# Kernel tuning notes

Hardware: AMD Instinct MI355X
Metric: run time of the kernel (lower is better)

Reference implementation:

```python
import jax, jax.numpy as jnp
import numpy as np

U, I, D = 100000, 200000, 64   # users, items, emb_size
N = U + I                      # total nodes
NNZ = 6400000                  # adjacency non-zeros
B = 4096                       # batch of (user,item) pairs
L = 3                          # n_layers


def setup_inputs() -> dict:
    key = jax.random.key(0)
    ks = jax.random.split(key, 11)
    s = 1.0 / np.sqrt(D)  # xavier-ish scale
    return {
        "user_emb_online": jax.random.normal(ks[0], (U, D), jnp.float32) * s,
        "item_emb_online": jax.random.normal(ks[1], (I, D), jnp.float32) * s,
        "user_emb_target": jax.random.normal(ks[2], (U, D), jnp.float32) * s,
        "item_emb_target": jax.random.normal(ks[3], (I, D), jnp.float32) * s,
        # normalized adjacency values (positive, roughly 1/deg scale)
        "adj_val": jax.random.uniform(ks[4], (NNZ,), jnp.float32) * (1.0 / 16.0),
        "pred_w": jax.random.normal(ks[5], (D, D), jnp.float32) * s,
        "pred_b": jnp.zeros((D,), jnp.float32),
        "adj_row": jax.random.randint(ks[6], (NNZ,), 0, N, dtype=jnp.int32),
        "adj_col": jax.random.randint(ks[7], (NNZ,), 0, N, dtype=jnp.int32),
        "user_idx": jax.random.randint(ks[8], (B,), 0, U, dtype=jnp.int32),
        "item_idx": jax.random.randint(ks[9], (B,), 0, I, dtype=jnp.int32),
    }


def _spmm(row, col, val, x):
    # sparse [N,N] @ dense [N,D] via gather + segment-sum
    return jax.ops.segment_sum(val[:, None] * x[col], row, num_segments=N)


def _lgcn_encode(user_emb, item_emb, row, col, val):
    ego = jnp.concatenate([user_emb, item_emb], axis=0)  # [N, D]
    acc = ego
    x = ego
    for _ in range(L):
        x = _spmm(row, col, val, x)
        acc = acc + x
    all_emb = acc / (L + 1)  # mean over stacked layer outputs
    return all_emb[:U], all_emb[U:]


def reference(user_emb_online, item_emb_online, user_emb_target, item_emb_target,
              adj_val, pred_w, pred_b, adj_row, adj_col, user_idx, item_idx):
    u_on_all, i_on_all = _lgcn_encode(user_emb_online, item_emb_online, adj_row, adj_col, adj_val)
    u_tg_all, i_tg_all = _lgcn_encode(user_emb_target, item_emb_target, adj_row, adj_col, adj_val)
    u_online = u_on_all[user_idx]   # [B, D]
    i_online = i_on_all[item_idx]
    u_target = u_tg_all[user_idx]
    i_target = i_tg_all[item_idx]
    u_pred = u_online @ pred_w.T + pred_b  # nn.Linear
    i_pred = i_online @ pred_w.T + pred_b
    return (u_pred, u_target, i_pred, i_target)
```

## Files before the change

### kernel.cpp

```cpp
#include <hip/hip_runtime.h>
#include <hip/hip_bf16.h>
#include <stdint.h>

#define U_N   100000
#define I_N   200000
#define NN    300000
#define DD    64
#define NNZ_N 6400000
#define BB    4096
#define CHUNK 4096
#define NB    ((NN + CHUNK - 1) / CHUNK)
#define NBK   74
#define EPB   4096
#define NSB   1184
#define SUBCAP 6656
#define BKCAP  94208
#define BKBLK  23
#define LBLK   48000

typedef unsigned short u16;
typedef unsigned int   u32;
typedef float vf2 __attribute__((ext_vector_type(2)));

__device__ __forceinline__ u16 f2bf(float f) {
    u32 u = __float_as_uint(f);
    u32 r = (u + 0x7FFFu + ((u >> 16) & 1u)) >> 16;
    return (u16)r;
}


#if __has_builtin(__builtin_amdgcn_cvt_pk_f32_fp8) && __has_builtin(__builtin_amdgcn_cvt_pk_fp8_f32)
#define FP8_HW 1
#else
#define FP8_HW 0
#endif

__device__ __forceinline__ u32 enc1_fp8(float f) {
    float af = fabsf(f);
    u32 s = (__float_as_uint(f) >> 31) << 7;
    if (af >= 0.015625f) {
        u32 au = __float_as_uint(af);
        u32 r = au + 0x7FFFFu + ((au >> 20) & 1u);
        u32 e = (r >> 23) - 120u;
        u32 m = (r >> 20) & 7u;
        if (e > 15u) { e = 15u; m = 6u; }
        return s | (e << 3) | m;
    } else {
        u32 q = (u32)__float2int_rn(af * 512.0f);
        return s | q;
    }
}

__device__ __forceinline__ u32 pack4_fp8(float a, float b, float c, float d) {
#if FP8_HW
    u32 w = 0;
    w = (u32)__builtin_amdgcn_cvt_pk_fp8_f32(a, b, (int)w, false);
    w = (u32)__builtin_amdgcn_cvt_pk_fp8_f32(c, d, (int)w, true);
    return w;
#else
    return enc1_fp8(a) | (enc1_fp8(b) << 8) | (enc1_fp8(c) << 16) | (enc1_fp8(d) << 24);
#endif
}

__device__ __forceinline__ float dec1_fp8(u32 b) {
    u32 s = (b & 0x80u) << 24;
    u32 e = (b >> 3) & 15u;
    u32 m = b & 7u;
    float mag = e ? __uint_as_float(((e + 120u) << 23) | (m << 20))
                  : (float)m * 0.001953125f;
    return __uint_as_float(__float_as_uint(mag) | s);
}

__device__ __forceinline__ void dec_fp8x4(u32 w, float* f) {
#if FP8_HW
    vf2 lo = __builtin_amdgcn_cvt_pk_f32_fp8((int)w, false);
    vf2 hi = __builtin_amdgcn_cvt_pk_f32_fp8((int)w, true);
    f[0] = lo[0]; f[1] = lo[1]; f[2] = hi[0]; f[3] = hi[1];
#else
    f[0] = dec1_fp8(w & 255u); f[1] = dec1_fp8((w >> 8) & 255u);
    f[2] = dec1_fp8((w >> 16) & 255u); f[3] = dec1_fp8(w >> 24);
#endif
}


__global__ void binit_k(int* __restrict__ bkt_cursor) {
    int t = threadIdx.x;
    if (t < NBK) bkt_cursor[t] = t * BKCAP;
}


__global__ __launch_bounds__(256) void p1_k(const int* __restrict__ adj_row,
                                            const int* __restrict__ adj_col,
                                            const float* __restrict__ adj_val,
                                            int* __restrict__ bkt_cursor,
                                            u32* __restrict__ bpk,
                                            float* __restrict__ bval) {
    __shared__ int lcnt[NBK];
    __shared__ int lbase[NBK];
    int base = blockIdx.x * EPB;
    for (int i = threadIdx.x; i < NBK; i += 256) lcnt[i] = 0;
    __syncthreads();
    u32 pk[16]; float vv[16]; int bb[16]; int rk[16];
#pragma unroll
    for (int j = 0; j < 16; j++) {
        int e = base + j * 256 + threadIdx.x;
        bb[j] = -1;
        if (e < NNZ_N) {
            int r = adj_row[e];
            int c = adj_col[e];
            vv[j] = adj_val[e];
            int b = r >> 12;
            pk[j] = ((u32)(r & 4095) << 19) | (u32)c;
            bb[j] = b;
            rk[j] = atomicAdd(&lcnt[b], 1);
        }
    }
    __syncthreads();
    for (int i = threadIdx.x; i < NBK; i += 256)
        lbase[i] = atomicAdd(&bkt_cursor[i], lcnt[i]);
    __syncthreads();
#pragma unroll
    for (int j = 0; j < 16; j++) {
        if (bb[j] >= 0) {
            int p = lbase[bb[j]] + rk[j];
            bpk[p]  = pk[j];
            bval[p] = vv[j];
        }
    }
}


__global__ __launch_bounds__(1024) void bhist_k(const int* __restrict__ bkt_cursor,
                                                const u32* __restrict__ bpk,
                                                int* __restrict__ cnt) {
    __shared__ int h[4096];
    int b = blockIdx.x;
    int base = b * BKCAP;
    int e1 = bkt_cursor[b];
    for (int j = threadIdx.x; j < 4096; j += 1024) h[j] = 0;
    __syncthreads();
    for (int i = base + threadIdx.x; i < e1; i += 1024)
        atomicAdd(&h[bpk[i] >> 19], 1);
    __syncthreads();
    int rb = b << 12;
    for (int j = threadIdx.x; j < 4096; j += 1024) {
        int idx = rb + j;
        if (idx < NN) cnt[idx] = h[j];
    }
}


__global__ void scan1_k(const int* __restrict__ cnt, int* __restrict__ bsums) {
    __shared__ int red[256];
    int base = blockIdx.x * CHUNK;
    int s = 0;
    for (int j = threadIdx.x; j < CHUNK; j += 256) {
        int idx = base + j;
        s += (idx < NN) ? cnt[idx] : 0;
    }
    red[threadIdx.x] = s;
    __syncthreads();
    for (int o = 128; o > 0; o >>= 1) {
        if (threadIdx.x < o) red[threadIdx.x] += red[threadIdx.x + o];
        __syncthreads();
    }
    if (threadIdx.x == 0) bsums[blockIdx.x] = red[0];
}

__global__ void scan2_k(int* __restrict__ bsums, int* __restrict__ row_ptr) {
    __shared__ int sh[128];
    int v = (threadIdx.x < NB) ? bsums[threadIdx.x] : 0;
    sh[threadIdx.x] = v;
    __syncthreads();
    for (int o = 1; o < 128; o <<= 1) {
        int t = (threadIdx.x >= o) ? sh[threadIdx.x - o] : 0;
        __syncthreads();
        sh[threadIdx.x] += t;
        __syncthreads();
    }
    if (threadIdx.x < NB) bsums[threadIdx.x] = sh[threadIdx.x] - v;
    if (threadIdx.x == 127) row_ptr[NN] = sh[127];
}

__global__ void scan3_k(const int* __restrict__ cnt, const int* __restrict__ bsums,
                        int* __restrict__ row_ptr) {
    __shared__ int tsum[256];
    int base = blockIdx.x * CHUNK;
    int loc[16];
    int s = 0;
#pragma unroll
    for (int j = 0; j < 16; j++) {
        int idx = base + threadIdx.x * 16 + j;
        int c = (idx < NN) ? cnt[idx] : 0;
        loc[j] = s;
        s += c;
    }
    tsum[threadIdx.x] = s;
    __syncthreads();
    int v = s;
    for (int o = 1; o < 256; o <<= 1) {
        int t = (threadIdx.x >= o) ? tsum[threadIdx.x - o] : 0;
        __syncthreads();
        tsum[threadIdx.x] += t;
        __syncthreads();
    }
    int texcl = tsum[threadIdx.x] - v;
    int boff = bsums[blockIdx.x];
#pragma unroll
    for (int j = 0; j < 16; j++) {
        int idx = base + threadIdx.x * 16 + j;
        if (idx < NN) row_ptr[idx] = boff + texcl + loc[j];
    }
}

__global__ void subinit_k(const int* __restrict__ row_ptr, int* __restrict__ sub_cursor) {
    int s = blockIdx.x * blockDim.x + threadIdx.x;
    if (s < NSB) {
        int r = s << 8;
        sub_cursor[s] = row_ptr[(r < NN) ? r : NN];
    }
}


__global__ __launch_bounds__(256) void p2r_k(const int* __restrict__ bkt_cursor,
                                             const u32* __restrict__ bpk,
                                             const float* __restrict__ bval,
                                             int* __restrict__ sub_cursor,
                                             int2* __restrict__ mid) {
    __shared__ int lcnt[16], lbase[16], sbase[16];
    __shared__ int2 stage[4096];
    int b = blockIdx.y;
    int e1 = bkt_cursor[b];
    int base = b * BKCAP + blockIdx.x * 4096;
    if (base >= e1) return;
    if (threadIdx.x < 16) lcnt[threadIdx.x] = 0;
    __syncthreads();
    u32 pk[16]; float vv[16]; int sb[16], rk[16];
#pragma unroll
    for (int j = 0; j < 16; j++) {
        int e = base + j * 256 + threadIdx.x;
        sb[j] = -1;
        if (e < e1) {
            pk[j] = bpk[e];
            vv[j] = bval[e];
            int s = (int)((pk[j] >> 27) & 15u);
            sb[j] = s;
            rk[j] = atomicAdd(&lcnt[s], 1);
        }
    }
    __syncthreads();
    if (threadIdx.x == 0) {
        int acc = 0;
#pragma unroll
        for (int s = 0; s < 16; s++) { sbase[s] = acc; acc += lcnt[s]; }
    }
    if (threadIdx.x < 16)
        lbase[threadIdx.x] = atomicAdd(&sub_cursor[b * 16 + threadIdx.x], lcnt[threadIdx.x]);
    __syncthreads();
#pragma unroll
    for (int j = 0; j < 16; j++)
        if (sb[j] >= 0)
            stage[sbase[sb[j]] + rk[j]] = make_int2((int)pk[j], __float_as_int(vv[j]));
    __syncthreads();
    for (int s = 0; s < 16; s++) {
        int c = lcnt[s], gb = lbase[s], lb = sbase[s];
        for (int i = threadIdx.x; i < c; i += 256)
            mid[gb + i] = stage[lb + i];
    }
}


__global__ __launch_bounds__(256) void p3_k(const int* __restrict__ row_ptr,
                                            const int2* __restrict__ mid,
                                            int2* __restrict__ edge_s) {
    __shared__ int rbase[256], rcur[256];
    __shared__ int2 stage[SUBCAP];
    int s = blockIdx.x;
    int r0 = s << 8;
    if (r0 >= NN) return;
    int r1 = min(r0 + 256, NN);
    int nr = r1 - r0;
    int ebase = row_ptr[r0];
    int eend  = row_ptr[r1];
    int cnt = eend - ebase;
    if (threadIdx.x < nr) {
        rbase[threadIdx.x] = row_ptr[r0 + threadIdx.x] - ebase;
        rcur[threadIdx.x] = 0;
    }
    __syncthreads();
    for (int i = threadIdx.x; i < cnt; i += 256) {
        int2 d = mid[ebase + i];
        u32 pk = (u32)d.x;
        int l = (int)((pk >> 19) & 255u);
        int pos = rbase[l] + atomicAdd(&rcur[l], 1);
        if (pos < SUBCAP) stage[pos] = make_int2((int)(pk & 0x7FFFFu), d.y);
    }
    __syncthreads();
    for (int i = threadIdx.x; i < cnt; i += 256) edge_s[ebase + i] = stage[i];
}


__global__ void mark_k(const int* __restrict__ row_ptr, const int2* __restrict__ edge_s,
                       const int* __restrict__ user_idx, const int* __restrict__ item_idx,
                       unsigned char* __restrict__ mark) {
    int wave = threadIdx.x >> 6;
    int lane = threadIdx.x & 63;
    int slot = blockIdx.x * 4 + wave;
    if (slot >= 2 * BB) return;
    int r = (slot < BB) ? user_idx[slot] : U_N + item_idx[slot - BB];
    if (lane == 0) mark[r] = 1;
    int e0 = row_ptr[r], e1 = row_ptr[r + 1];
    for (int e = e0 + lane; e < e1; e += 64) mark[edge_s[e].x] = 1;
}

__global__ void compact_k(const unsigned char* __restrict__ mark,
                          int* __restrict__ list2, int* __restrict__ nlist) {
    int i = blockIdx.x * 256 + threadIdx.x;
    int lane = threadIdx.x & 63;
    int m = (i < NN) ? (int)mark[i] : 0;
    unsigned long long b = __ballot(m != 0);
    int pre = __popcll(b & ((1ull << lane) - 1ull));
    int tot = __popcll(b);
    int base = 0;
    if (lane == 0 && tot) base = atomicAdd(nlist, tot);
    base = __shfl(base, 0);
    if (m) list2[base + pre] = i;
}


__global__ void pack1_k(const float* __restrict__ ue_on, const float* __restrict__ ie_on,
                        const float* __restrict__ ue_tg, const float* __restrict__ ie_tg,
                        unsigned char* __restrict__ x0f) {
    int tid = blockIdx.x * blockDim.x + threadIdx.x;
    int n = tid >> 4;
    int t = tid & 15;
    if (n >= NN) return;
    const float* src;
    int soff;
    if (t < 8) {
        soff = t * 8;
        src = (n < U_N) ? ue_on + (size_t)n * 64 : ie_on + (size_t)(n - U_N) * 64;
    } else {
        soff = (t - 8) * 8;
        src = (n < U_N) ? ue_tg + (size_t)n * 64 : ie_tg + (size_t)(n - U_N) * 64;
    }
    float4 f0 = *(const float4*)(src + soff);
    float4 f1 = *(const float4*)(src + soff + 4);
    uint2 o;
    o.x = pack4_fp8(f0.x, f0.y, f0.z, f0.w);
    o.y = pack4_fp8(f1.x, f1.y, f1.z, f1.w);
    *(uint2*)(x0f + (size_t)n * 128 + t * 8) = o;
}


struct acc8 { float a[8]; };

__device__ __forceinline__ void red8(acc8& A) {
#pragma unroll
    for (int k = 0; k < 8; k++) {
        A.a[k] += __shfl_xor(A.a[k], 16);
        A.a[k] += __shfl_xor(A.a[k], 32);
    }
}

__global__ __launch_bounds__(256) void spmm1_k(const int* __restrict__ row_ptr,
                                               const int2* __restrict__ edge_s,
                                               const unsigned char* __restrict__ x0f,
                                               u16* __restrict__ y) {
    int lane = threadIdx.x & 63;
    int t = lane & 15, g = lane >> 4;
    int r = blockIdx.x * 4 + (threadIdx.x >> 6);
    if (r >= NN) return;
    int e0 = row_ptr[r], e1 = row_ptr[r + 1];
    int d = e1 - e0;
    acc8 A;
#pragma unroll
    for (int k = 0; k < 8; k++) A.a[k] = 0.f;
    const unsigned char* xt = x0f + t * 8;

    int2 ed[8];
    uint2 pv[8];
#pragma unroll
    for (int q = 0; q < 8; q++) { ed[q] = make_int2(0, 0); pv[q] = make_uint2(0u, 0u); }
#pragma unroll
    for (int q = 0; q < 8; q++) {
        int j = g + 4 * q;
        if (j < d) ed[q] = edge_s[e0 + j];
    }
#pragma unroll
    for (int q = 0; q < 8; q++) {
        int j = g + 4 * q;
        if (j < d) pv[q] = *(const uint2*)(xt + (size_t)(u32)ed[q].x * 128);
    }
#pragma unroll
    for (int q = 0; q < 8; q++) {
        float v = __int_as_float(ed[q].y);
        float f[8];
        dec_fp8x4(pv[q].x, f);
        dec_fp8x4(pv[q].y, f + 4);
#pragma unroll
        for (int k = 0; k < 8; k++) A.a[k] += v * f[k];
    }
    for (int e = e0 + 32 + g * 4; e < e1; e += 16) {
        int m = e1 - e;
#pragma unroll
        for (int k = 0; k < 4; k++) {
            if (k < m) {
                int2 dd = edge_s[e + k];
                float v = __int_as_float(dd.y);
                uint2 p = *(const uint2*)(xt + (size_t)(u32)dd.x * 128);
                float f[8];
                dec_fp8x4(p.x, f);
                dec_fp8x4(p.y, f + 4);
#pragma unroll
                for (int q = 0; q < 8; q++) A.a[q] += v * f[q];
            }
        }
    }
    red8(A);
    if (g == 0) {
        uint4 o;
        o.x = ((u32)f2bf(A.a[1]) << 16) | (u32)f2bf(A.a[0]);
        o.y = ((u32)f2bf(A.a[3]) << 16) | (u32)f2bf(A.a[2]);
        o.z = ((u32)f2bf(A.a[5]) << 16) | (u32)f2bf(A.a[4]);
        o.w = ((u32)f2bf(A.a[7]) << 16) | (u32)f2bf(A.a[6]);
        *(uint4*)(y + (size_t)r * 128 + t * 8) = o;
    }
}

__device__ __forceinline__ void rg16_core(const int2* __restrict__ edge_s,
                                          const u16* __restrict__ x,
                                          int t, int g, int e0, int e1, acc8& A) {
#pragma unroll
    for (int k = 0; k < 8; k++) A.a[k] = 0.f;
    const u16* xt = x + t * 8;
    int d = e1 - e0;

    int2 ed[8];
    uint4 pv[8];
#pragma unroll
    for (int q = 0; q < 8; q++) { ed[q] = make_int2(0, 0); pv[q] = make_uint4(0u, 0u, 0u, 0u); }
#pragma unroll
    for (int q = 0; q < 8; q++) {
        int j = g + 4 * q;
        if (j < d) ed[q] = edge_s[e0 + j];
    }
#pragma unroll
    for (int q = 0; q < 8; q++) {
        int j = g + 4 * q;
        if (j < d) pv[q] = *(const uint4*)(xt + (size_t)(u32)ed[q].x * 128);
    }
#pragma unroll
    for (int q = 0; q < 8; q++) {
        float v = __int_as_float(ed[q].y);
        A.a[0] += v * __uint_as_float(pv[q].x << 16);
        A.a[1] += v * __uint_as_float(pv[q].x & 0xFFFF0000u);
        A.a[2] += v * __uint_as_float(pv[q].y << 16);
        A.a[3] += v * __uint_as_float(pv[q].y & 0xFFFF0000u);
        A.a[4] += v * __uint_as_float(pv[q].z << 16);
        A.a[5] += v * __uint_as_float(pv[q].z & 0xFFFF0000u);
        A.a[6] += v * __uint_as_float(pv[q].w << 16);
        A.a[7] += v * __uint_as_float(pv[q].w & 0xFFFF0000u);
    }
    for (int e = e0 + 32 + g * 4; e < e1; e += 16) {
        int m = e1 - e;
#pragma unroll
        for (int k = 0; k < 4; k++) {
            if (k < m) {
                int2 dd = edge_s[e + k];
                float v = __int_as_float(dd.y);
                uint4 p = *(const uint4*)(xt + (size_t)(u32)dd.x * 128);
                A.a[0] += v * __uint_as_float(p.x << 16);
                A.a[1] += v * __uint_as_float(p.x & 0xFFFF0000u);
                A.a[2] += v * __uint_as_float(p.y << 16);
                A.a[3] += v * __uint_as_float(p.y & 0xFFFF0000u);
                A.a[4] += v * __uint_as_float(p.z << 16);
                A.a[5] += v * __uint_as_float(p.z & 0xFFFF0000u);
                A.a[6] += v * __uint_as_float(p.w << 16);
                A.a[7] += v * __uint_as_float(p.w & 0xFFFF0000u);
            }
        }
    }
    red8(A);
}

__global__ __launch_bounds__(256) void spmm_list_k(const int* __restrict__ row_ptr,
                                                   const int2* __restrict__ edge_s,
                                                   const u16* __restrict__ x,
                                                   u16* __restrict__ y,
                                                   const int* __restrict__ list2,
                                                   const int* __restrict__ nlist) {
    int lane = threadIdx.x & 63;
    int t = lane & 15, g = lane >> 4;
    int slot = blockIdx.x * 4 + (threadIdx.x >> 6);
    if (slot >= *nlist) return;
    int r = list2[slot];
    acc8 A;
    rg16_core(edge_s, x, t, g, row_ptr[r], row_ptr[r + 1], A);
    if (g == 0) {
        uint4 o;
        o.x = ((u32)f2bf(A.a[1]) << 16) | (u32)f2bf(A.a[0]);
        o.y = ((u32)f2bf(A.a[3]) << 16) | (u32)f2bf(A.a[2]);
        o.z = ((u32)f2bf(A.a[5]) << 16) | (u32)f2bf(A.a[4]);
        o.w = ((u32)f2bf(A.a[7]) << 16) | (u32)f2bf(A.a[6]);
        *(uint4*)(y + (size_t)r * 128 + t * 8) = o;
    }
}

__global__ __launch_bounds__(256) void spmm_last_k(const int* __restrict__ row_ptr,
                                                   const int2* __restrict__ edge_s,
                                                   const u16* __restrict__ x,
                                                   const int* __restrict__ user_idx,
                                                   const int* __restrict__ item_idx,
                                                   float* __restrict__ out_acc) {
    int lane = threadIdx.x & 63;
    int t = lane & 15, g = lane >> 4;
    int slot = blockIdx.x * 4 + (threadIdx.x >> 6);
    if (slot >= 2 * BB) return;
    int r = (slot < BB) ? user_idx[slot] : U_N + item_idx[slot - BB];
    acc8 A;
    rg16_core(edge_s, x, t, g, row_ptr[r], row_ptr[r + 1], A);
    if (g == 0) {
        float4* p0 = (float4*)(out_acc + (size_t)slot * 128 + t * 8);
        float4 c0 = p0[0], c1 = p0[1];
        c0.x += A.a[0]; c0.y += A.a[1]; c0.z += A.a[2]; c0.w += A.a[3];
        c1.x += A.a[4]; c1.y += A.a[5]; c1.z += A.a[6]; c1.w += A.a[7];
        p0[0] = c0; p0[1] = c1;
    }
}


__global__ void init_acc_k(const int* __restrict__ user_idx, const int* __restrict__ item_idx,
                           const float* __restrict__ ue_on, const float* __restrict__ ie_on,
                           const float* __restrict__ ue_tg, const float* __restrict__ ie_tg,
                           float* __restrict__ out_acc) {
    int t = blockIdx.x * blockDim.x + threadIdx.x;
    int slot = t >> 5;
    int j = t & 31;
    if (slot >= 2 * BB) return;
    int node = (slot < BB) ? user_idx[slot] : U_N + item_idx[slot - BB];
    const float* src;
    int soff, doff;
    if (j < 16) {
        soff = j * 4; doff = j * 4;
        src = (node < U_N) ? ue_on + (size_t)node * 64 : ie_on + (size_t)(node - U_N) * 64;
    } else {
        soff = (j - 16) * 4; doff = 64 + (j - 16) * 4;
        src = (node < U_N) ? ue_tg + (size_t)node * 64 : ie_tg + (size_t)(node - U_N) * 64;
    }
    float4 f = *(const float4*)(src + soff);
    *(float4*)(out_acc + (size_t)slot * 128 + doff) = f;
}

__global__ void gadd_k(const int* __restrict__ user_idx, const int* __restrict__ item_idx,
                       const u16* __restrict__ x, float* __restrict__ out_acc) {
    int t = blockIdx.x * blockDim.x + threadIdx.x;
    int slot = t >> 6;
    int l = t & 63;
    if (slot >= 2 * BB) return;
    int node = (slot < BB) ? user_idx[slot] : U_N + item_idx[slot - BB];
    u32 p = *(const u32*)(x + (size_t)node * 128 + (l << 1));
    float fx = __uint_as_float(p << 16);
    float fy = __uint_as_float(p & 0xFFFF0000u);
    float2* q = (float2*)(out_acc + (size_t)slot * 128) + l;
    float2 cur = *q;
    cur.x += fx; cur.y += fy;
    *q = cur;
}


__global__ __launch_bounds__(256) void pred_k(const float* __restrict__ out_acc,
                                              const float* __restrict__ W,
                                              const float* __restrict__ bias,
                                              float* __restrict__ out) {
    __shared__ float wld[64 * 65];
    __shared__ float uld[4 * 64];
    int j = threadIdx.x & 63;
    int rl = threadIdx.x >> 6;
    for (int i = threadIdx.x; i < 4096; i += 256) {
        int jj = i >> 6, kk = i & 63;
        wld[kk * 65 + jj] = W[i];
    }
    int slot = blockIdx.x * 4 + rl;
    uld[rl * 64 + j] = out_acc[(size_t)slot * 128 + j] * 0.25f;
    float tv = out_acc[(size_t)slot * 128 + 64 + j] * 0.25f;
    size_t tdst = (slot < BB) ? (size_t)BB * 64 + (size_t)slot * 64 + j
                              : (size_t)3 * BB * 64 + (size_t)(slot - BB) * 64 + j;
    out[tdst] = tv;
    __syncthreads();
    float acc = bias[j];
#pragma unroll
    for (int k = 0; k < 64; k++) acc += uld[rl * 64 + k] * wld[k * 65 + j];
    size_t dst = (slot < BB) ? (size_t)slot * 64 + j
                             : (size_t)2 * BB * 64 + (size_t)(slot - BB) * 64 + j;
    out[dst] = acc;
}


extern "C" void kernel_launch(void* const* d_in, const int* in_sizes, int n_in,
                              void* d_out, int out_size, void* d_ws, size_t ws_size,
                              hipStream_t stream) {
    const float* ue_on = (const float*)d_in[0];
    const float* ie_on = (const float*)d_in[1];
    const float* ue_tg = (const float*)d_in[2];
    const float* ie_tg = (const float*)d_in[3];
    const float* adj_val = (const float*)d_in[4];
    const float* pred_w = (const float*)d_in[5];
    const float* pred_b = (const float*)d_in[6];
    const int* adj_row = (const int*)d_in[7];
    const int* adj_col = (const int*)d_in[8];
    const int* user_idx = (const int*)d_in[9];
    const int* item_idx = (const int*)d_in[10];
    float* out = (float*)d_out;

    char* ws = (char*)d_ws;
    size_t off = 0;
    auto alloc = [&](size_t bytes) -> char* {
        char* p = ws + off;
        off = (off + bytes + 255) & ~(size_t)255;
        return p;
    };
    int*   cnt        = (int*)alloc((size_t)NN * 4);
    int*   row_ptr    = (int*)alloc((size_t)(NN + 1) * 4);
    int*   bsums      = (int*)alloc(256 * 4);
    int*   bkt_cursor = (int*)alloc(256 * 4);
    int*   sub_cursor = (int*)alloc((size_t)NSB * 4);
    unsigned char* mark = (unsigned char*)alloc((size_t)NN);
    int*   list2      = (int*)alloc((size_t)NN * 4);
    int*   nlist      = (int*)alloc(256 * 4);
    int2*  edge_s     = (int2*)alloc((size_t)NNZ_N * 8);
    u16*   x_a        = (u16*)alloc((size_t)NN * 128 * 2);
    u16*   x_b        = (u16*)alloc((size_t)NN * 128 * 2);
    float* out_acc    = (float*)alloc((size_t)2 * BB * 128 * 4);

    u32*   bpk  = (u32*)x_a;
    unsigned char* x0f = (unsigned char*)x_a;
    float* bval = (float*)x_b;
    int2*  mid  = edge_s;

    (void)n_in; (void)in_sizes; (void)out_size; (void)ws_size;

    hipMemsetAsync(mark, 0, (size_t)NN, stream);
    hipMemsetAsync(nlist, 0, 4, stream);
    binit_k<<<1, 128, 0, stream>>>(bkt_cursor);
    p1_k<<<(NNZ_N + EPB - 1) / EPB, 256, 0, stream>>>(adj_row, adj_col, adj_val, bkt_cursor, bpk, bval);
    bhist_k<<<NBK, 1024, 0, stream>>>(bkt_cursor, bpk, cnt);
    scan1_k<<<NB, 256, 0, stream>>>(cnt, bsums);
    scan2_k<<<1, 128, 0, stream>>>(bsums, row_ptr);
    scan3_k<<<NB, 256, 0, stream>>>(cnt, bsums, row_ptr);
    subinit_k<<<(NSB + 255) / 256, 256, 0, stream>>>(row_ptr, sub_cursor);
    p2r_k<<<dim3(BKBLK, NBK), 256, 0, stream>>>(bkt_cursor, bpk, bval, sub_cursor, mid);
    p3_k<<<NSB, 256, 0, stream>>>(row_ptr, mid, edge_s);

    mark_k<<<(2 * BB) / 4, 256, 0, stream>>>(row_ptr, edge_s, user_idx, item_idx, mark);
    compact_k<<<(NN + 255) / 256, 256, 0, stream>>>(mark, list2, nlist);

    pack1_k<<<(NN * 16 + 255) / 256, 256, 0, stream>>>(ue_on, ie_on, ue_tg, ie_tg, x0f);
    init_acc_k<<<(2 * BB * 32) / 256, 256, 0, stream>>>(user_idx, item_idx, ue_on, ie_on, ue_tg, ie_tg, out_acc);

    spmm1_k<<<NN / 4, 256, 0, stream>>>(row_ptr, edge_s, x0f, x_b);
    gadd_k<<<(2 * BB * 64) / 256, 256, 0, stream>>>(user_idx, item_idx, x_b, out_acc);
    spmm_list_k<<<LBLK, 256, 0, stream>>>(row_ptr, edge_s, x_b, x_a, list2, nlist);
    gadd_k<<<(2 * BB * 64) / 256, 256, 0, stream>>>(user_idx, item_idx, x_a, out_acc);
    spmm_last_k<<<(2 * BB) / 4, 256, 0, stream>>>(row_ptr, edge_s, x_a, user_idx, item_idx, out_acc);

    pred_k<<<(2 * BB) / 4, 256, 0, stream>>>(out_acc, pred_w, pred_b, out);
}
```

Baseline: 791.7 us.

## Gather layer-2 inputs from an FP8 copy and fuse small setup kernels

```diff
diff --git a/kernel.cpp b/kernel.cpp
--- a/kernel.cpp
+++ b/kernel.cpp
@@ -83,9 +83,12 @@
 }
 
 
-__global__ void binit_k(int* __restrict__ bkt_cursor) {
-    int t = threadIdx.x;
-    if (t < NBK) bkt_cursor[t] = t * BKCAP;
+__global__ void setup_k(unsigned char* __restrict__ mark, int* __restrict__ nlist,
+                        int* __restrict__ bkt_cursor) {
+    int tid = blockIdx.x * 256 + threadIdx.x;
+    if (tid < NN / 4) ((u32*)mark)[tid] = 0;
+    if (tid < NBK) bkt_cursor[tid] = tid * BKCAP;
+    if (tid == NN / 4) nlist[0] = 0;
 }
 
 
@@ -183,7 +186,7 @@
 }
 
 __global__ void scan3_k(const int* __restrict__ cnt, const int* __restrict__ bsums,
-                        int* __restrict__ row_ptr) {
+                        int* __restrict__ row_ptr, int* __restrict__ sub_cursor) {
     __shared__ int tsum[256];
     int base = blockIdx.x * CHUNK;
     int loc[16];
@@ -209,15 +212,11 @@
 #pragma unroll
     for (int j = 0; j < 16; j++) {
         int idx = base + threadIdx.x * 16 + j;
-        if (idx < NN) row_ptr[idx] = boff + texcl + loc[j];
-    }
-}
-
-__global__ void subinit_k(const int* __restrict__ row_ptr, int* __restrict__ sub_cursor) {
-    int s = blockIdx.x * blockDim.x + threadIdx.x;
-    if (s < NSB) {
-        int r = s << 8;
-        sub_cursor[s] = row_ptr[(r < NN) ? r : NN];
+        if (idx < NN) {
+            int val = boff + texcl + loc[j];
+            row_ptr[idx] = val;
+            if ((idx & 255) == 0) sub_cursor[idx >> 8] = val;
+        }
     }
 }
 
@@ -363,20 +362,13 @@
     }
 }
 
-__global__ __launch_bounds__(256) void spmm1_k(const int* __restrict__ row_ptr,
-                                               const int2* __restrict__ edge_s,
-                                               const unsigned char* __restrict__ x0f,
-                                               u16* __restrict__ y) {
-    int lane = threadIdx.x & 63;
-    int t = lane & 15, g = lane >> 4;
-    int r = blockIdx.x * 4 + (threadIdx.x >> 6);
-    if (r >= NN) return;
-    int e0 = row_ptr[r], e1 = row_ptr[r + 1];
+__device__ __forceinline__ void rg8_core(const int2* __restrict__ edge_s,
+                                         const unsigned char* __restrict__ xf,
+                                         int t, int g, int e0, int e1, acc8& A) {
+#pragma unroll
+    for (int k = 0; k < 8; k++) A.a[k] = 0.f;
+    const unsigned char* xt = xf + t * 8;
     int d = e1 - e0;
-    acc8 A;
-#pragma unroll
-    for (int k = 0; k < 8; k++) A.a[k] = 0.f;
-    const unsigned char* xt = x0f + t * 8;
 
     int2 ed[8];
     uint2 pv[8];
@@ -390,7 +382,7 @@
 #pragma unroll
     for (int q = 0; q < 8; q++) {
         int j = g + 4 * q;
-        if (j < d) pv[q] = *(const uint2*)(xt + (size_t)(u32)ed[q].x * 128);
+        if (j < d) pv[q] = *(const uint2*)(xt + (size_t)((u32)ed[q].x * 128u));
     }
 #pragma unroll
     for (int q = 0; q < 8; q++) {
@@ -408,7 +400,7 @@
             if (k < m) {
                 int2 dd = edge_s[e + k];
                 float v = __int_as_float(dd.y);
-                uint2 p = *(const uint2*)(xt + (size_t)(u32)dd.x * 128);
+                uint2 p = *(const uint2*)(xt + (size_t)((u32)dd.x * 128u));
                 float f[8];
                 dec_fp8x4(p.x, f);
                 dec_fp8x4(p.y, f + 4);
@@ -418,6 +410,19 @@
         }
     }
     red8(A);
+}
+
+__global__ __launch_bounds__(256) void spmm1_k(const int* __restrict__ row_ptr,
+                                               const int2* __restrict__ edge_s,
+                                               const unsigned char* __restrict__ x0f,
+                                               u16* __restrict__ y,
+                                               unsigned char* __restrict__ yf) {
+    int lane = threadIdx.x & 63;
+    int t = lane & 15, g = lane >> 4;
+    int r = blockIdx.x * 4 + (threadIdx.x >> 6);
+    if (r >= NN) return;
+    acc8 A;
+    rg8_core(edge_s, x0f, t, g, row_ptr[r], row_ptr[r + 1], A);
     if (g == 0) {
         uint4 o;
         o.x = ((u32)f2bf(A.a[1]) << 16) | (u32)f2bf(A.a[0]);
@@ -425,6 +430,10 @@
         o.z = ((u32)f2bf(A.a[5]) << 16) | (u32)f2bf(A.a[4]);
         o.w = ((u32)f2bf(A.a[7]) << 16) | (u32)f2bf(A.a[6]);
         *(uint4*)(y + (size_t)r * 128 + t * 8) = o;
+        uint2 of;
+        of.x = pack4_fp8(A.a[0], A.a[1], A.a[2], A.a[3]);
+        of.y = pack4_fp8(A.a[4], A.a[5], A.a[6], A.a[7]);
+        *(uint2*)(yf + (size_t)r * 128 + t * 8) = of;
     }
 }
 
@@ -486,7 +495,7 @@
 
 __global__ __launch_bounds__(256) void spmm_list_k(const int* __restrict__ row_ptr,
                                                    const int2* __restrict__ edge_s,
-                                                   const u16* __restrict__ x,
+                                                   const unsigned char* __restrict__ x1f,
                                                    u16* __restrict__ y,
                                                    const int* __restrict__ list2,
                                                    const int* __restrict__ nlist) {
@@ -496,7 +505,7 @@
     if (slot >= *nlist) return;
     int r = list2[slot];
     acc8 A;
-    rg16_core(edge_s, x, t, g, row_ptr[r], row_ptr[r + 1], A);
+    rg8_core(edge_s, x1f, t, g, row_ptr[r], row_ptr[r + 1], A);
     if (g == 0) {
         uint4 o;
         o.x = ((u32)f2bf(A.a[1]) << 16) | (u32)f2bf(A.a[0]);
@@ -521,6 +530,15 @@
     acc8 A;
     rg16_core(edge_s, x, t, g, row_ptr[r], row_ptr[r + 1], A);
     if (g == 0) {
+        uint4 p = *(const uint4*)(x + (size_t)r * 128 + t * 8);
+        A.a[0] += __uint_as_float(p.x << 16);
+        A.a[1] += __uint_as_float(p.x & 0xFFFF0000u);
+        A.a[2] += __uint_as_float(p.y << 16);
+        A.a[3] += __uint_as_float(p.y & 0xFFFF0000u);
+        A.a[4] += __uint_as_float(p.z << 16);
+        A.a[5] += __uint_as_float(p.z & 0xFFFF0000u);
+        A.a[6] += __uint_as_float(p.w << 16);
+        A.a[7] += __uint_as_float(p.w & 0xFFFF0000u);
         float4* p0 = (float4*)(out_acc + (size_t)slot * 128 + t * 8);
         float4 c0 = p0[0], c1 = p0[1];
         c0.x += A.a[0]; c0.y += A.a[1]; c0.z += A.a[2]; c0.w += A.a[3];
@@ -635,20 +653,18 @@
 
     u32*   bpk  = (u32*)x_a;
     unsigned char* x0f = (unsigned char*)x_a;
+    unsigned char* x1f = (unsigned char*)x_a + (size_t)NN * 128;
     float* bval = (float*)x_b;
     int2*  mid  = edge_s;
 
     (void)n_in; (void)in_sizes; (void)out_size; (void)ws_size;
 
-    hipMemsetAsync(mark, 0, (size_t)NN, stream);
-    hipMemsetAsync(nlist, 0, 4, stream);
-    binit_k<<<1, 128, 0, stream>>>(bkt_cursor);
+    setup_k<<<294, 256, 0, stream>>>(mark, nlist, bkt_cursor);
     p1_k<<<(NNZ_N + EPB - 1) / EPB, 256, 0, stream>>>(adj_row, adj_col, adj_val, bkt_cursor, bpk, bval);
     bhist_k<<<NBK, 1024, 0, stream>>>(bkt_cursor, bpk, cnt);
     scan1_k<<<NB, 256, 0, stream>>>(cnt, bsums);
     scan2_k<<<1, 128, 0, stream>>>(bsums, row_ptr);
-    scan3_k<<<NB, 256, 0, stream>>>(cnt, bsums, row_ptr);
-    subinit_k<<<(NSB + 255) / 256, 256, 0, stream>>>(row_ptr, sub_cursor);
+    scan3_k<<<NB, 256, 0, stream>>>(cnt, bsums, row_ptr, sub_cursor);
     p2r_k<<<dim3(BKBLK, NBK), 256, 0, stream>>>(bkt_cursor, bpk, bval, sub_cursor, mid);
     p3_k<<<NSB, 256, 0, stream>>>(row_ptr, mid, edge_s);
 
@@ -658,11 +674,10 @@
     pack1_k<<<(NN * 16 + 255) / 256, 256, 0, stream>>>(ue_on, ie_on, ue_tg, ie_tg, x0f);
     init_acc_k<<<(2 * BB * 32) / 256, 256, 0, stream>>>(user_idx, item_idx, ue_on, ie_on, ue_tg, ie_tg, out_acc);
 
-    spmm1_k<<<NN / 4, 256, 0, stream>>>(row_ptr, edge_s, x0f, x_b);
+    spmm1_k<<<NN / 4, 256, 0, stream>>>(row_ptr, edge_s, x0f, x_b, x1f);
     gadd_k<<<(2 * BB * 64) / 256, 256, 0, stream>>>(user_idx, item_idx, x_b, out_acc);
-    spmm_list_k<<<LBLK, 256, 0, stream>>>(row_ptr, edge_s, x_b, x_a, list2, nlist);
-    gadd_k<<<(2 * BB * 64) / 256, 256, 0, stream>>>(user_idx, item_idx, x_a, out_acc);
-    spmm_last_k<<<(2 * BB) / 4, 256, 0, stream>>>(row_ptr, edge_s, x_a, user_idx, item_idx, out_acc);
+    spmm_list_k<<<LBLK, 256, 0, stream>>>(row_ptr, edge_s, x1f, x_b, list2, nlist);
+    spmm_last_k<<<(2 * BB) / 4, 256, 0, stream>>>(row_ptr, edge_s, x_b, user_idx, item_idx, out_acc);
 
     pred_k<<<(2 * BB) / 4, 256, 0, stream>>>(out_acc, pred_w, pred_b, out);
 }
```

After: 756.7 us. 4.4% less time.
